# Kernel tuning notes

Hardware: AMD Instinct MI355X
Metric: run time of the kernel (lower is better)

## Reference

```python
import jax, jax.numpy as jnp
import numpy as np
from jax import lax

B, C_IN, IMG, P = 8, 320, 64, 2
H = W = IMG // P            # 32
N = H * W                   # 1024 tokens
DIM = 128 * P * P           # 512
DEPTH, HEADS, DH = 6, 8, 64
INNER = HEADS * DH          # 512
MLP = 512
EPS = 1e-5


def layernorm(x, g, b):
    mu = x.mean(-1, keepdims=True)
    var = ((x - mu) ** 2).mean(-1, keepdims=True)
    return (x - mu) * lax.rsqrt(var + EPS) * g + b


def conv3x3(x, w, b):
    y = lax.conv_general_dilated(x, w, (1, 1), 'SAME',
                                 dimension_numbers=('NCHW', 'OIHW', 'NCHW'))
    return y + b[None, :, None, None]


def posemb_sincos_2d(h, w, dim, temperature=10000.0):
    y, x = jnp.meshgrid(jnp.arange(h, dtype=jnp.float32),
                        jnp.arange(w, dtype=jnp.float32), indexing='ij')
    omega = jnp.arange(dim // 4, dtype=jnp.float32) / (dim // 4 - 1)
    omega = 1.0 / (temperature ** omega)
    y = y.reshape(-1)[:, None] * omega[None, :]
    x = x.reshape(-1)[:, None] * omega[None, :]
    return jnp.concatenate([jnp.sin(x), jnp.cos(x), jnp.sin(y), jnp.cos(y)], axis=1)


def prepare_attn_mask(mask):
    # attn mask allows position pairs where either row or col token is marked.
    f = 64 // H
    m = (mask == 1)
    r = m.reshape(-1, H, f, W, f).any(axis=(2, 4)).reshape(-1, N)  # [M, N] bool
    return r[:, :, None] | r[:, None, :]                            # [M, N, N]


def setup_inputs() -> dict:
    key = jax.random.key(0)
    ks = jax.random.split(key, 24)
    s = 0.02
    d = dict(
        img=jax.random.normal(ks[0], (B, C_IN, IMG, IMG), jnp.float32),
        mask=jax.random.randint(ks[1], (DEPTH * B, 64, 64), 0, 2, jnp.int32),
        conv1_w=jax.random.normal(ks[2], (128, C_IN, 3, 3), jnp.float32) * s,
        conv1_b=jnp.zeros((128,), jnp.float32),
        ln_p_g=jnp.ones((DIM,), jnp.float32), ln_p_b=jnp.zeros((DIM,), jnp.float32),
        proj_w=jax.random.normal(ks[3], (DIM, DIM), jnp.float32) * s,
        proj_b=jnp.zeros((DIM,), jnp.float32),
        ln_q_g=jnp.ones((DIM,), jnp.float32), ln_q_b=jnp.zeros((DIM,), jnp.float32),
        attn_ln_g=jnp.ones((DEPTH, DIM), jnp.float32),
        attn_ln_b=jnp.zeros((DEPTH, DIM), jnp.float32),
        wqkv=jax.random.normal(ks[4], (DEPTH, DIM, 3 * INNER), jnp.float32) * s,
        wo=jax.random.normal(ks[5], (DEPTH, INNER, DIM), jnp.float32) * s,
        ff_ln_g=jnp.ones((DEPTH, DIM), jnp.float32),
        ff_ln_b=jnp.zeros((DEPTH, DIM), jnp.float32),
        w1=jax.random.normal(ks[6], (DEPTH, DIM, MLP), jnp.float32) * s,
        b1=jnp.zeros((DEPTH, MLP), jnp.float32),
        w2=jax.random.normal(ks[7], (DEPTH, MLP, DIM), jnp.float32) * s,
        b2=jnp.zeros((DEPTH, DIM), jnp.float32),
        conv2_w=jax.random.normal(ks[8], (C_IN, 128, 3, 3), jnp.float32) * s,
        conv2_b=jnp.zeros((C_IN,), jnp.float32),
    )
    return d


def reference(img, mask, conv1_w, conv1_b, ln_p_g, ln_p_b, proj_w, proj_b,
              ln_q_g, ln_q_b, attn_ln_g, attn_ln_b, wqkv, wo,
              ff_ln_g, ff_ln_b, w1, b1, w2, b2, conv2_w, conv2_b):
    am = prepare_attn_mask(mask).reshape(DEPTH, B, N, N)  # per-layer masks

    # patch embed: conv -> rearrange 'b c (h p1) (w p2) -> b (h w) (p1 p2 c)'
    y = conv3x3(img, conv1_w, conv1_b)                           # [B,128,64,64]
    y = y.reshape(B, 128, H, P, W, P).transpose(0, 2, 4, 3, 5, 1)
    y = y.reshape(B, N, P * P * 128)                             # [B,N,512]
    x = layernorm(y, ln_p_g, ln_p_b) @ proj_w + proj_b
    x = layernorm(x, ln_q_g, ln_q_b)
    x = x + posemb_sincos_2d(H, W, DIM).astype(x.dtype)

    scale = DH ** -0.5
    for i in range(DEPTH):
        xn = layernorm(x, attn_ln_g[i], attn_ln_b[i])
        qkv = xn @ wqkv[i]                                       # [B,N,3*INNER]
        q, k, v = jnp.split(qkv, 3, axis=-1)
        q, k, v = (t.reshape(B, N, HEADS, DH).transpose(0, 2, 1, 3)
                   for t in (q, k, v))
        dots = jnp.einsum('bhid,bhjd->bhij', q, k) * scale
        min_val = lax.stop_gradient(dots.min())
        dots = jnp.where(am[i][:, None, :, :], dots, min_val)
        attn = jax.nn.softmax(dots, axis=-1)
        o = jnp.einsum('bhij,bhjd->bhid', attn, v)
        o = o.transpose(0, 2, 1, 3).reshape(B, N, INNER) @ wo[i]
        x = o + x
        h = layernorm(x, ff_ln_g[i], ff_ln_b[i]) @ w1[i] + b1[i]
        x = jax.nn.gelu(h, approximate=False) @ w2[i] + b2[i] + x

    # 'b (h w) (p1 p2 c) -> b c (h p1) (w p2)' then conv
    z = x.reshape(B, H, W, P, P, 128).transpose(0, 5, 1, 3, 2, 4)
    z = z.reshape(B, 128, IMG, IMG)
    return conv3x3(z, conv2_w, conv2_b)
```

## Files before the change

### kernel.cpp

```cpp
#include <hip/hip_runtime.h>
#include <hip/hip_bf16.h>
#include <math.h>

typedef __attribute__((ext_vector_type(8))) short short8;
typedef __attribute__((ext_vector_type(4))) float f32x4;
typedef unsigned short u16;
typedef unsigned int u32;

#define DEV __device__ __forceinline__

DEV float bf2f(u16 u){ u32 x = ((u32)u)<<16; return __builtin_bit_cast(float, x); }
DEV u16 f2bf(float f){ u32 x = __builtin_bit_cast(u32, f); return (u16)((x + 0x7FFFu + ((x>>16)&1u))>>16); }
DEV f32x4 mfma16(short8 a, short8 b, f32x4 c){ return __builtin_amdgcn_mfma_f32_16x16x32_bf16(a,b,c,0,0,0); }
DEV void gload16(const void* g, void* l){
  __builtin_amdgcn_global_load_lds((const __attribute__((address_space(1))) void*)g,
                                   (__attribute__((address_space(3))) void*)l, 16, 0, 0);
}
DEV u32 fkey(float f){ u32 b = __builtin_bit_cast(u32, f); return (b & 0x80000000u) ? ~b : (b ^ 0x80000000u); }
DEV float funkey(u32 k){ u32 b = (k & 0x80000000u) ? (k ^ 0x80000000u) : ~k; return __builtin_bit_cast(float, b); }

static constexpr size_t O_PROJW = 0;
static constexpr size_t O_QKVW  = O_PROJW + 524288;
static constexpr size_t O_WOW   = O_QKVW + 9437184;
static constexpr size_t O_W1W   = O_WOW + 3145728;
static constexpr size_t O_W2W   = O_W1W + 3145728;
static constexpr size_t O_C1W   = O_W2W + 3145728;
static constexpr size_t O_C2W   = O_C1W + 737280;
static constexpr size_t O_RA    = O_C2W + 737280;
static constexpr size_t O_RB    = O_RA + 22302720;
static constexpr size_t O_X     = O_RB + 25165824;
static constexpr size_t O_D     = O_X + 16777216;
static constexpr size_t O_F     = O_D + 8388608;
static constexpr size_t O_RM    = O_F + 8388608;
static constexpr size_t O_MIN   = O_RM + 49152;
static constexpr size_t WS_NEED = O_MIN + 256;

__global__ __launch_bounds__(256) void k_transpose_bf(const float* __restrict__ src, u16* __restrict__ dst, int K, int N){
  __shared__ float tile[32][33];
  const int k0 = blockIdx.x*32, n0 = blockIdx.y*32;
  src += (size_t)blockIdx.z*K*N; dst += (size_t)blockIdx.z*K*N;
  const int c = threadIdx.x & 31, r4 = threadIdx.x >> 5;
  for(int r=r4; r<32; r+=8) tile[r][c] = src[(size_t)(k0+r)*N + n0+c];
  __syncthreads();
  for(int r=r4; r<32; r+=8) dst[(size_t)(n0+r)*K + k0+c] = f2bf(tile[c][r]);
}

__global__ __launch_bounds__(256) void k_convw(const float* __restrict__ src, u16* __restrict__ dst, int OC, int IC){
  int idx = blockIdx.x*256 + threadIdx.x;
  int total = OC*IC*9;
  if(idx >= total) return;
  int oc = idx/(IC*9); int rem = idx - oc*IC*9; int tap = rem/IC; int ic = rem - tap*IC;
  dst[idx] = f2bf(src[(size_t)(oc*IC+ic)*9 + tap]);
}

__global__ __launch_bounds__(256) void k_pad_img(const float* __restrict__ img, u16* __restrict__ pcl){
  const int by = blockIdx.x; const int b = by>>6, y = by&63; const int c0 = blockIdx.y*64;
  __shared__ float t[64][65];
  const int tx = threadIdx.x & 63, tz = threadIdx.x >> 6;
  for(int ci=tz; ci<64; ci+=4) t[ci][tx] = img[(((size_t)b*320 + c0+ci)*64 + y)*64 + tx];
  __syncthreads();
  for(int x=tz; x<64; x+=4) pcl[(((size_t)b*66 + y+1)*66 + (x+1))*320 + c0 + tx] = f2bf(t[tx][x]);
}

__global__ __launch_bounds__(256) void k_pad_tok(const float* __restrict__ x, u16* __restrict__ pcl){
  int idx = blockIdx.x*256 + threadIdx.x;
  const int c = idx & 127; int r = idx >> 7; const int xx = r & 63; r >>= 6; const int yy = r & 63; const int b = r >> 6;
  const int n = (yy>>1)*32 + (xx>>1); const int f = (yy&1)*256 + (xx&1)*128 + c;
  pcl[(((size_t)b*66 + yy+1)*66 + xx+1)*128 + c] = f2bf(x[((size_t)b*1024 + n)*512 + f]);
}

__global__ __launch_bounds__(256) void k_rmask(const int* __restrict__ mask, unsigned char* __restrict__ rm){
  int idx = blockIdx.x*256 + threadIdx.x;
  if(idx >= 48*1024) return;
  const int m = idx >> 10, n = idx & 1023; const int h = n>>5, w = n&31;
  const int* mp = mask + ((size_t)m*64 + h*2)*64 + w*2;
  rm[idx] = (unsigned char)((mp[0]==1) | (mp[1]==1) | (mp[64]==1) | (mp[65]==1));
}

__global__ __launch_bounds__(256) void k_vt(const u16* __restrict__ v, u16* __restrict__ vt){
  const int nt = blockIdx.x, bh = blockIdx.y;
  __shared__ u16 t[64][72];
  const int tid = threadIdx.x;
  const int i = tid>>2, cq = tid&3;
  const u16* src = v + ((size_t)bh*1024 + nt*64 + i)*64 + cq*16;
  const short8 s0 = *(const short8*)src;
  const short8 s1 = *(const short8*)(src+8);
  #pragma unroll
  for(int e=0;e<8;e++){ t[cq*16+e][i] = (u16)s0[e]; t[cq*16+8+e][i] = (u16)s1[e]; }
  __syncthreads();
  short8 o0, o1;
  #pragma unroll
  for(int e=0;e<8;e++){ o0[e] = (short)t[i][cq*16+e]; o1[e] = (short)t[i][cq*16+8+e]; }
  u16* dst = vt + (size_t)bh*65536 + (size_t)i*1024 + nt*64 + cq*16;
  *(short8*)dst = o0;
  *(short8*)(dst+8) = o1;
}

__global__ __launch_bounds__(256) void k_ln_bf(const float* __restrict__ in, const float* __restrict__ gw,
                                               const float* __restrict__ bw, u16* __restrict__ out){
  const int tok = blockIdx.x*4 + (threadIdx.x>>6);
  const int lane = threadIdx.x & 63;
  const float* rp = in + (size_t)tok*512 + lane*8;
  const float4 a = *(const float4*)rp;
  const float4 b = *(const float4*)(rp+4);
  float s  = a.x+a.y+a.z+a.w + b.x+b.y+b.z+b.w;
  float sq = a.x*a.x+a.y*a.y+a.z*a.z+a.w*a.w + b.x*b.x+b.y*b.y+b.z*b.z+b.w*b.w;
  #pragma unroll
  for(int off=1; off<64; off<<=1){ s += __shfl_xor(s,off); sq += __shfl_xor(sq,off); }
  const float mu = s*(1.f/512.f);
  const float rs = rsqrtf(fmaxf(sq*(1.f/512.f) - mu*mu, 0.f) + 1e-5f);
  const float4 g0 = *(const float4*)(gw + lane*8);
  const float4 g1 = *(const float4*)(gw + lane*8 + 4);
  const float4 b0 = *(const float4*)(bw + lane*8);
  const float4 b1 = *(const float4*)(bw + lane*8 + 4);
  short8 o8;
  o8[0]=f2bf((a.x-mu)*rs*g0.x+b0.x); o8[1]=f2bf((a.y-mu)*rs*g0.y+b0.y);
  o8[2]=f2bf((a.z-mu)*rs*g0.z+b0.z); o8[3]=f2bf((a.w-mu)*rs*g0.w+b0.w);
  o8[4]=f2bf((b.x-mu)*rs*g1.x+b1.x); o8[5]=f2bf((b.y-mu)*rs*g1.y+b1.y);
  o8[6]=f2bf((b.z-mu)*rs*g1.z+b1.z); o8[7]=f2bf((b.w-mu)*rs*g1.w+b1.w);
  *(short8*)(out + (size_t)tok*512 + lane*8) = o8;
}

__global__ __launch_bounds__(256) void k_lnq_pos(const float* __restrict__ in, const float* __restrict__ gw,
                                                 const float* __restrict__ bw, float* __restrict__ out){
  const int tok = blockIdx.x*4 + (threadIdx.x>>6);
  const int lane = threadIdx.x & 63;
  const float* rp = in + (size_t)tok*512 + lane*8;
  const float4 a = *(const float4*)rp;
  const float4 b = *(const float4*)(rp+4);
  float s  = a.x+a.y+a.z+a.w + b.x+b.y+b.z+b.w;
  float sq = a.x*a.x+a.y*a.y+a.z*a.z+a.w*a.w + b.x*b.x+b.y*b.y+b.z*b.z+b.w*b.w;
  #pragma unroll
  for(int off=1; off<64; off<<=1){ s += __shfl_xor(s,off); sq += __shfl_xor(sq,off); }
  const float mu = s*(1.f/512.f);
  const float rs = rsqrtf(fmaxf(sq*(1.f/512.f) - mu*mu, 0.f) + 1e-5f);
  const int n = tok & 1023; const int yy = n>>5, xx = n&31;
  const int f0 = lane*8; const int sec = f0>>7;
  const float coord = (sec<2) ? (float)xx : (float)yy;
  const float vv[8] = {a.x,a.y,a.z,a.w,b.x,b.y,b.z,b.w};
  float ov[8];
  #pragma unroll
  for(int j=0;j<8;j++){
    const int f = f0+j; const int qq = f & 127;
    const float om = __expf(-(float)qq * (9.2103403719761836f/127.f));
    const float arg = coord * om;
    const float pe = (sec&1) ? __cosf(arg) : __sinf(arg);
    ov[j] = (vv[j]-mu)*rs*gw[f] + bw[f] + pe;
  }
  float* op = out + (size_t)tok*512 + f0;
  *(float4*)op = (float4){ov[0],ov[1],ov[2],ov[3]};
  *(float4*)(op+4) = (float4){ov[4],ov[5],ov[6],ov[7]};
}

template<int EPI, int CONVC>
__global__ __launch_bounds__(256, 4)
void k_gemm(const u16* __restrict__ A, const u16* __restrict__ Wt,
            const float* __restrict__ bias, void* __restrict__ outp,
            const float* __restrict__ resid, int M, int N, int Kd)
{
  __shared__ u16 Ald[2][4096];
  __shared__ u16 Bld[2][4096];
  const int tid = threadIdx.x, lane = tid & 63, wv = tid >> 6;
  const int lr = lane & 15, g = lane >> 4;
  const int m0 = blockIdx.x * 64, n0 = blockIdx.y * 64;
  const int wm = (wv >> 1) * 32, wn = (wv & 1) * 32;
  const int srow = tid >> 3;
  const int sc  = (tid & 7) ^ (srow & 7);
  int b0=0, yy0=0;
  if constexpr (CONVC != 0){ b0 = m0>>12; yy0 = (m0>>6)&63; }
  const u16* arow0p; const u16* arow1p;
  if constexpr (CONVC != 0){
    arow0p = A; arow1p = A;
  } else {
    arow0p = A + (size_t)(m0+srow)*Kd + sc*8;
    arow1p = A + (size_t)(m0+srow+32)*Kd + sc*8;
  }
  const u16* brow0p = Wt + (size_t)(n0+srow)*Kd + sc*8;
  const u16* brow1p = Wt + (size_t)(n0+srow+32)*Kd + sc*8;

  f32x4 acc[2][2];
  #pragma unroll
  for(int i=0;i<2;i++)
    #pragma unroll
    for(int j=0;j<2;j++) acc[i][j] = (f32x4){0.f,0.f,0.f,0.f};

  const int nIter = Kd >> 6;
  int cur = 0;

  auto stage = [&](int kt, int buf){
    const int k0 = kt << 6;
    const u16 *ga0, *ga1;
    if constexpr (CONVC != 0){
      const int tap = k0 / CONVC;
      const int ic0 = k0 - tap*CONVC;
      const int ky = tap/3, kx = tap - 3*(tap/3);
      const size_t rb0 = ((size_t)((b0*66 + yy0+ky)*66 + kx))*CONVC + ic0 + sc*8;
      ga0 = A + rb0 + (size_t)(srow)*CONVC;
      ga1 = A + rb0 + (size_t)(srow+32)*CONVC;
    } else {
      ga0 = arow0p + k0;
      ga1 = arow1p + k0;
    }
    gload16(ga0, &Ald[buf][tid*8]);
    gload16(ga1, &Ald[buf][2048 + tid*8]);
    gload16(brow0p + k0, &Bld[buf][tid*8]);
    gload16(brow1p + k0, &Bld[buf][2048 + tid*8]);
  };

  stage(0, 0);
  for(int kt=0; kt<nIter; ++kt){
    __syncthreads();
    if(kt+1 < nIter) stage(kt+1, cur^1);
    short8 af[2][2], bg[2][2];
    #pragma unroll
    for(int mi=0;mi<2;mi++)
      #pragma unroll
      for(int kk=0;kk<2;kk++){
        const int R = wm + mi*16 + lr;
        const int Rn = wn + mi*16 + lr;
        const int c = kk*4 + g;
        af[mi][kk] = *(const short8*)&Ald[cur][R*64 + ((c ^ (R&7))<<3)];
        bg[mi][kk] = *(const short8*)&Bld[cur][Rn*64 + ((c ^ (Rn&7))<<3)];
      }
    #pragma unroll
    for(int mi=0;mi<2;mi++)
      #pragma unroll
      for(int nj=0;nj<2;nj++)
        #pragma unroll
        for(int kk=0;kk<2;kk++)
          acc[mi][nj] = mfma16(af[mi][kk], bg[nj][kk], acc[mi][nj]);
    cur ^= 1;
  }

  #pragma unroll
  for(int mi=0;mi<2;mi++){
    #pragma unroll
    for(int nj=0;nj<2;nj++){
      #pragma unroll
      for(int r=0;r<4;r++){
        const int mrow = m0 + wm + mi*16 + g*4 + r;
        const int ncol = n0 + wn + nj*16 + lr;
        float val = acc[mi][nj][r];
        if constexpr (EPI==0 || EPI==3 || EPI==4 || EPI==5 || EPI==6)
          val += bias[ncol];
        if constexpr (EPI==0){
          ((float*)outp)[(size_t)mrow*512 + ncol] = val;
        } else if constexpr (EPI==1){
          const int sec = ncol >> 9, rem = ncol & 511;
          const int head = rem >> 6, d = rem & 63;
          const int b = mrow >> 10, t = mrow & 1023;
          ((u16*)outp)[(size_t)sec*4194304 + ((size_t)((b*8+head)*1024 + t))*64 + d] = f2bf(val);
        } else if constexpr (EPI==2 || EPI==4){
          const size_t idx = (size_t)mrow*512 + ncol;
          ((float*)outp)[idx] = resid[idx] + val;
        } else if constexpr (EPI==3){
          const float gl = 0.5f * val * (1.f + erff(val * 0.70710678118654752f));
          ((u16*)outp)[(size_t)mrow*512 + ncol] = f2bf(gl);
        } else if constexpr (EPI==5){
          const int b = mrow>>12; const int rr = mrow&4095; const int y = rr>>6; const int xx = rr&63;
          const size_t pidx = ((size_t)(b*1024 + (y>>1)*32 + (xx>>1)))*512 + (y&1)*256 + (xx&1)*128 + ncol;
          ((float*)outp)[pidx] = val;
        } else if constexpr (EPI==6){
          const int b = mrow>>12; const int rr = mrow&4095; const int y = rr>>6; const int xx = rr&63;
          ((float*)outp)[(((size_t)(b*320 + ncol))*64 + y)*64 + xx] = val;
        }
      }
    }
  }
}

__global__ __launch_bounds__(256, 4)
void k_attn_minmax(const u16* __restrict__ q, const u16* __restrict__ k, u32* __restrict__ keys, int layer){
  const int id = blockIdx.x;
  const int qt = (id>>3)&15;
  const int bh = ((id&7)<<3) | (id>>7);
  __shared__ u16 Kld[2][4096];
  __shared__ float redn[4], redx[4];
  const int tid = threadIdx.x, lane = tid & 63, wv = tid >> 6;
  const int lr = lane & 15, g = lane >> 4;
  const u16* qp = q + ((size_t)bh*1024 + qt*64 + wv*16 + lr)*64;
  const short8 qa0 = *(const short8*)(qp + g*8);
  const short8 qa1 = *(const short8*)(qp + 32 + g*8);
  const u16* kbase = k + (size_t)bh*65536;
  const int srow = tid>>3, scs = lane&7;
  const int scg = scs ^ (srow&7);
  const int srow2 = srow + 32;
  const int scg2 = scs ^ (srow2&7);
  float mn = 3.0e38f, mx = -3.0e38f;
  gload16(kbase + (size_t)srow*64 + scg*8, &Kld[0][wv*512]);
  gload16(kbase + (size_t)srow2*64 + scg2*8, &Kld[0][2048 + wv*512]);
  int cur = 0;
  for(int jt=0; jt<16; ++jt){
    __syncthreads();
    if(jt < 15){
      const int j1 = (jt+1)*64;
      gload16(kbase + (size_t)(j1+srow)*64 + scg*8, &Kld[cur^1][wv*512]);
      gload16(kbase + (size_t)(j1+srow2)*64 + scg2*8, &Kld[cur^1][2048 + wv*512]);
    }
    #pragma unroll
    for(int c=0;c<4;c++){
      const int rr = c*16 + lr;
      const short8 kb0 = *(const short8*)&Kld[cur][rr*64 + ((g ^ (rr&7))<<3)];
      const short8 kb1 = *(const short8*)&Kld[cur][rr*64 + (((g+4) ^ (rr&7))<<3)];
      f32x4 s4 = (f32x4){0.f,0.f,0.f,0.f};
      s4 = mfma16(qa0, kb0, s4);
      s4 = mfma16(qa1, kb1, s4);
      mn = fminf(mn, fminf(fminf(s4[0],s4[1]), fminf(s4[2],s4[3])));
      mx = fmaxf(mx, fmaxf(fmaxf(s4[0],s4[1]), fmaxf(s4[2],s4[3])));
    }
    cur ^= 1;
  }
  mn *= 0.125f; mx *= 0.125f;
  #pragma unroll
  for(int off=32; off; off>>=1){
    mn = fminf(mn, __shfl_down(mn, off));
    mx = fmaxf(mx, __shfl_down(mx, off));
  }
  if(lane==0){ redn[wv] = mn; redx[wv] = mx; }
  __syncthreads();
  if(tid==0){
    atomicMin(keys + layer,     fkey(fminf(fminf(redn[0],redn[1]), fminf(redn[2],redn[3]))));
    atomicMax(keys + 8 + layer, fkey(fmaxf(fmaxf(redx[0],redx[1]), fmaxf(redx[2],redx[3]))));
  }
}

__global__ __launch_bounds__(256, 4)
void k_attn(const u16* __restrict__ q, const u16* __restrict__ k, const u16* __restrict__ vt,
            const unsigned char* __restrict__ rm, const u32* __restrict__ keys,
            u16* __restrict__ o, int layer){
  const int id = blockIdx.x;
  const int qt = (id>>3)&15;
  const int bh = ((id&7)<<3) | (id>>7);
  const int b = bh>>3, h = bh&7;
  __shared__ u16 Kld[2][4096];
  __shared__ u16 Vtld[2][4096];
  __shared__ u16 Pld[4][1024];
  const int tid = threadIdx.x, lane = tid & 63, wv = tid >> 6;
  const int lr = lane & 15, g = lane >> 4;
  const u16* qp = q + ((size_t)bh*1024 + qt*64 + wv*16 + lr)*64;
  const short8 qa0 = *(const short8*)(qp + g*8);
  const short8 qa1 = *(const short8*)(qp + 32 + g*8);
  const float L2E = 1.44269504088896f;
  const float SC = 0.125f * L2E;
  float mnv = funkey(keys[layer]);
  float mxv = funkey(keys[8+layer]);
  if(!(mnv >= -1e38f && mnv <= 1e38f)) mnv = 0.f;
  if(!(mxv >= -1e38f && mxv <= 1e38f)) mxv = 0.f;
  const float minvE = mnv * L2E;
  const float ME    = mxv * L2E;
  const unsigned char* rmp = rm + (size_t)(layer*8 + b)*1024;
  bool rrow[4];
  #pragma unroll
  for(int r=0;r<4;r++) rrow[r] = rmp[qt*64 + wv*16 + g*4 + r] != 0;
  float lrun[4] = {0.f,0.f,0.f,0.f};
  f32x4 accd[4];
  #pragma unroll
  for(int d=0;d<4;d++) accd[d] = (f32x4){0.f,0.f,0.f,0.f};
  const u16* kbase = k + (size_t)bh*65536;
  const u16* vtbase = vt + (size_t)bh*65536;
  const int srow = tid>>3, scs = lane&7;
  const int scg = scs ^ (srow&7);
  const int srow2 = srow + 32;
  const int scg2 = scs ^ (srow2&7);
  gload16(kbase + (size_t)srow*64 + scg*8, &Kld[0][wv*512]);
  gload16(kbase + (size_t)srow2*64 + scg2*8, &Kld[0][2048 + wv*512]);
  gload16(vtbase + (size_t)srow*1024 + scg*8, &Vtld[0][wv*512]);
  gload16(vtbase + (size_t)srow2*1024 + scg2*8, &Vtld[0][2048 + wv*512]);
  int cur = 0;
  for(int jt=0; jt<16; ++jt){
    const int j0 = jt*64;
    __syncthreads();
    if(jt < 15){
      const int j1 = j0 + 64;
      gload16(kbase + (size_t)(j1+srow)*64 + scg*8, &Kld[cur^1][wv*512]);
      gload16(kbase + (size_t)(j1+srow2)*64 + scg2*8, &Kld[cur^1][2048 + wv*512]);
      gload16(vtbase + (size_t)srow*1024 + j1 + scg*8, &Vtld[cur^1][wv*512]);
      gload16(vtbase + (size_t)srow2*1024 + j1 + scg2*8, &Vtld[cur^1][2048 + wv*512]);
    }
    float p4[4][4];
    #pragma unroll
    for(int c=0;c<4;c++){
      const int rr = c*16 + lr;
      const short8 kb0 = *(const short8*)&Kld[cur][rr*64 + ((g ^ (rr&7))<<3)];
      const short8 kb1 = *(const short8*)&Kld[cur][rr*64 + (((g+4) ^ (rr&7))<<3)];
      f32x4 s4 = (f32x4){0.f,0.f,0.f,0.f};
      s4 = mfma16(qa0, kb0, s4);
      s4 = mfma16(qa1, kb1, s4);
      const bool colok = rmp[j0 + rr] != 0;
      #pragma unroll
      for(int r=0;r<4;r++){
        const float vl = (rrow[r] | colok) ? s4[r]*SC : minvE;
        p4[c][r] = exp2f(fmaxf(vl - ME, -120.f));
      }
    }
    #pragma unroll
    for(int r=0;r<4;r++)
      lrun[r] += (p4[0][r]+p4[1][r]) + (p4[2][r]+p4[3][r]);
    #pragma unroll
    for(int c=0;c<4;c++)
      #pragma unroll
      for(int r=0;r<4;r++){
        const int ql = g*4+r, cl = c*16+lr;
        Pld[wv][ql*64 + ((((cl>>3) ^ (ql&7))<<3) | (cl&7))] = f2bf(p4[c][r]);
      }
    asm volatile("s_waitcnt lgkmcnt(0)" ::: "memory");
    __builtin_amdgcn_sched_barrier(0);
    const short8 pa0 = *(const short8*)&Pld[wv][lr*64 + ((g ^ (lr&7))<<3)];
    const short8 pa1 = *(const short8*)&Pld[wv][lr*64 + (((g+4) ^ (lr&7))<<3)];
    #pragma unroll
    for(int d=0;d<4;d++){
      const int rr = d*16 + lr;
      const short8 vb0 = *(const short8*)&Vtld[cur][rr*64 + ((g ^ (rr&7))<<3)];
      const short8 vb1 = *(const short8*)&Vtld[cur][rr*64 + (((g+4) ^ (rr&7))<<3)];
      accd[d] = mfma16(pa0, vb0, accd[d]);
      accd[d] = mfma16(pa1, vb1, accd[d]);
    }
    cur ^= 1;
  }
  float inv[4];
  #pragma unroll
  for(int r=0;r<4;r++){
    float ls = lrun[r];
    ls += __shfl_xor(ls,1); ls += __shfl_xor(ls,2);
    ls += __shfl_xor(ls,4); ls += __shfl_xor(ls,8);
    inv[r] = 1.f / ls;
  }
  #pragma unroll
  for(int d=0;d<4;d++)
    #pragma unroll
    for(int r=0;r<4;r++){
      const int qrow = qt*64 + wv*16 + g*4 + r;
      o[((size_t)b*1024 + qrow)*512 + h*64 + d*16 + lr] = f2bf(accd[d][r] * inv[r]);
    }
}

extern "C" void kernel_launch(void* const* d_in, const int* in_sizes, int n_in,
                              void* d_out, int out_size, void* d_ws, size_t ws_size,
                              hipStream_t stream)
{
  const float* img     = (const float*)d_in[0];
  const int*   mask    = (const int*)d_in[1];
  const float* conv1_w = (const float*)d_in[2];
  const float* conv1_b = (const float*)d_in[3];
  const float* ln_p_g  = (const float*)d_in[4];
  const float* ln_p_b  = (const float*)d_in[5];
  const float* proj_w  = (const float*)d_in[6];
  const float* proj_b  = (const float*)d_in[7];
  const float* ln_q_g  = (const float*)d_in[8];
  const float* ln_q_b  = (const float*)d_in[9];
  const float* attn_ln_g = (const float*)d_in[10];
  const float* attn_ln_b = (const float*)d_in[11];
  const float* wqkv    = (const float*)d_in[12];
  const float* wo      = (const float*)d_in[13];
  const float* ff_ln_g = (const float*)d_in[14];
  const float* ff_ln_b = (const float*)d_in[15];
  const float* w1      = (const float*)d_in[16];
  const float* b1      = (const float*)d_in[17];
  const float* w2      = (const float*)d_in[18];
  const float* b2      = (const float*)d_in[19];
  const float* conv2_w = (const float*)d_in[20];
  const float* conv2_b = (const float*)d_in[21];

  if(ws_size < WS_NEED) return;
  char* ws = (char*)d_ws;
  u16* projWt = (u16*)(ws + O_PROJW);
  u16* qkvWt  = (u16*)(ws + O_QKVW);
  u16* woWt   = (u16*)(ws + O_WOW);
  u16* w1Wt   = (u16*)(ws + O_W1W);
  u16* w2Wt   = (u16*)(ws + O_W2W);
  u16* c1Wt   = (u16*)(ws + O_C1W);
  u16* c2Wt   = (u16*)(ws + O_C2W);
  u16* pcl    = (u16*)(ws + O_RA);
  float* tmpf = (float*)(ws + O_RA);
  u16* vtb    = (u16*)(ws + O_RA);
  float* patches = (float*)(ws + O_RB);
  u16* qkvb   = (u16*)(ws + O_RB);
  float* xbuf = (float*)(ws + O_X);
  u16* xnbf   = (u16*)(ws + O_D);
  u16* obf    = (u16*)(ws + O_F);
  unsigned char* rmb = (unsigned char*)(ws + O_RM);
  u32* minbuf = (u32*)(ws + O_MIN);

  hipMemsetAsync(ws + O_MIN, 0xFF, 32, stream);
  hipMemsetAsync(ws + O_MIN + 32, 0, 32, stream);
  hipMemsetAsync(ws + O_RA, 0, 22302720, stream);

  k_transpose_bf<<<dim3(16,16,1),256,0,stream>>>(proj_w, projWt, 512, 512);
  k_transpose_bf<<<dim3(16,48,6),256,0,stream>>>(wqkv,   qkvWt,  512, 1536);
  k_transpose_bf<<<dim3(16,16,6),256,0,stream>>>(wo,     woWt,   512, 512);
  k_transpose_bf<<<dim3(16,16,6),256,0,stream>>>(w1,     w1Wt,   512, 512);
  k_transpose_bf<<<dim3(16,16,6),256,0,stream>>>(w2,     w2Wt,   512, 512);
  k_convw<<<1440,256,0,stream>>>(conv1_w, c1Wt, 128, 320);
  k_convw<<<1440,256,0,stream>>>(conv2_w, c2Wt, 320, 128);
  k_rmask<<<192,256,0,stream>>>(mask, rmb);

  k_pad_img<<<dim3(512,5),256,0,stream>>>(img, pcl);
  k_gemm<5,320><<<dim3(512,2),256,0,stream>>>(pcl, c1Wt, conv1_b, patches, nullptr, 32768, 128, 2880);
  k_ln_bf<<<2048,256,0,stream>>>(patches, ln_p_g, ln_p_b, xnbf);
  k_gemm<0,0><<<dim3(128,8),256,0,stream>>>(xnbf, projWt, proj_b, tmpf, nullptr, 8192, 512, 512);
  k_lnq_pos<<<2048,256,0,stream>>>(tmpf, ln_q_g, ln_q_b, xbuf);

  const u16* qb = qkvb;
  const u16* kb = qkvb + 4194304;
  const u16* vb = qkvb + 8388608;
  for(int i=0;i<6;i++){
    k_ln_bf<<<2048,256,0,stream>>>(xbuf, attn_ln_g + i*512, attn_ln_b + i*512, xnbf);
    k_gemm<1,0><<<dim3(128,24),256,0,stream>>>(xnbf, qkvWt + (size_t)i*1536*512, nullptr, qkvb, nullptr, 8192, 1536, 512);
    k_vt<<<dim3(16,64),256,0,stream>>>(vb, vtb);
    k_attn_minmax<<<1024,256,0,stream>>>(qb, kb, minbuf, i);
    k_attn<<<1024,256,0,stream>>>(qb, kb, vtb, rmb, minbuf, obf, i);
    k_gemm<2,0><<<dim3(128,8),256,0,stream>>>(obf, woWt + (size_t)i*512*512, nullptr, xbuf, xbuf, 8192, 512, 512);
    k_ln_bf<<<2048,256,0,stream>>>(xbuf, ff_ln_g + i*512, ff_ln_b + i*512, xnbf);
    k_gemm<3,0><<<dim3(128,8),256,0,stream>>>(xnbf, w1Wt + (size_t)i*512*512, b1 + i*512, obf, nullptr, 8192, 512, 512);
    k_gemm<4,0><<<dim3(128,8),256,0,stream>>>(obf, w2Wt + (size_t)i*512*512, b2 + i*512, xbuf, xbuf, 8192, 512, 512);
  }

  hipMemsetAsync(ws + O_RA, 0, 8921088, stream);
  k_pad_tok<<<16384,256,0,stream>>>(xbuf, pcl);
  k_gemm<6,128><<<dim3(512,5),256,0,stream>>>(pcl, c2Wt, conv2_b, d_out, nullptr, 32768, 320, 1152);
}
```

Baseline: 1.070 ms.

## Use bit-packed row masks and transposed QK^T MFMA in attention softmax

The token mask is packed into 64-bit ballot words, so the attention kernel reads column and row validity as bits instead of per-element byte loads. The QK^T MFMA operands are swapped so each lane holds a query row across key columns. This lets the row sum be accumulated in a single scalar and lets P be written to LDS as packed bf16 pairs via v_cvt_pk_bf16_f32. s_setprio is raised around the MFMAs in both attention kernels. The changes are meant to cut mask loads, scalar converts and LDS stores in the softmax inner loop, at the cost of trickier lane/swizzle indexing that must stay consistent with the PV MFMA layout.

```diff
diff --git a/kernel.cpp b/kernel.cpp
--- a/kernel.cpp
+++ b/kernel.cpp
@@ -6,6 +6,7 @@
 typedef __attribute__((ext_vector_type(4))) float f32x4;
 typedef unsigned short u16;
 typedef unsigned int u32;
+typedef unsigned long long u64;
 
 #define DEV __device__ __forceinline__
 
@@ -18,6 +19,7 @@
 }
 DEV u32 fkey(float f){ u32 b = __builtin_bit_cast(u32, f); return (b & 0x80000000u) ? ~b : (b ^ 0x80000000u); }
 DEV float funkey(u32 k){ u32 b = (k & 0x80000000u) ? (k ^ 0x80000000u) : ~k; return __builtin_bit_cast(float, b); }
+DEV u32 cvtpk(float lo, float hi){ u32 d; asm("v_cvt_pk_bf16_f32 %0, %1, %2" : "=v"(d) : "v"(lo), "v"(hi)); return d; }
 
 static constexpr size_t O_PROJW = 0;
 static constexpr size_t O_QKVW  = O_PROJW + 524288;
@@ -33,7 +35,8 @@
 static constexpr size_t O_F     = O_D + 8388608;
 static constexpr size_t O_RM    = O_F + 8388608;
 static constexpr size_t O_MIN   = O_RM + 49152;
-static constexpr size_t WS_NEED = O_MIN + 256;
+static constexpr size_t O_RMB   = O_MIN + 256;
+static constexpr size_t WS_NEED = O_RMB + 8192;
 
 __global__ __launch_bounds__(256) void k_transpose_bf(const float* __restrict__ src, u16* __restrict__ dst, int K, int N){
   __shared__ float tile[32][33];
@@ -69,12 +72,15 @@
   pcl[(((size_t)b*66 + yy+1)*66 + xx+1)*128 + c] = f2bf(x[((size_t)b*1024 + n)*512 + f]);
 }
 
-__global__ __launch_bounds__(256) void k_rmask(const int* __restrict__ mask, unsigned char* __restrict__ rm){
+__global__ __launch_bounds__(256) void k_rmask(const int* __restrict__ mask, unsigned char* __restrict__ rm,
+                                               u64* __restrict__ rmbits){
   int idx = blockIdx.x*256 + threadIdx.x;
-  if(idx >= 48*1024) return;
   const int m = idx >> 10, n = idx & 1023; const int h = n>>5, w = n&31;
   const int* mp = mask + ((size_t)m*64 + h*2)*64 + w*2;
-  rm[idx] = (unsigned char)((mp[0]==1) | (mp[1]==1) | (mp[64]==1) | (mp[65]==1));
+  const int v = (mp[0]==1) | (mp[1]==1) | (mp[64]==1) | (mp[65]==1);
+  rm[idx] = (unsigned char)v;
+  const u64 bm = __ballot(v);
+  if((threadIdx.x & 63) == 0) rmbits[idx>>6] = bm;
 }
 
 __global__ __launch_bounds__(256) void k_vt(const u16* __restrict__ v, u16* __restrict__ vt){
@@ -303,8 +309,10 @@
       const short8 kb0 = *(const short8*)&Kld[cur][rr*64 + ((g ^ (rr&7))<<3)];
       const short8 kb1 = *(const short8*)&Kld[cur][rr*64 + (((g+4) ^ (rr&7))<<3)];
       f32x4 s4 = (f32x4){0.f,0.f,0.f,0.f};
+      __builtin_amdgcn_s_setprio(1);
       s4 = mfma16(qa0, kb0, s4);
       s4 = mfma16(qa1, kb1, s4);
+      __builtin_amdgcn_s_setprio(0);
       mn = fminf(mn, fminf(fminf(s4[0],s4[1]), fminf(s4[2],s4[3])));
       mx = fmaxf(mx, fmaxf(fmaxf(s4[0],s4[1]), fmaxf(s4[2],s4[3])));
     }
@@ -326,7 +334,7 @@
 
 __global__ __launch_bounds__(256, 4)
 void k_attn(const u16* __restrict__ q, const u16* __restrict__ k, const u16* __restrict__ vt,
-            const unsigned char* __restrict__ rm, const u32* __restrict__ keys,
+            const u64* __restrict__ rmbits, const u32* __restrict__ keys,
             u16* __restrict__ o, int layer){
   const int id = blockIdx.x;
   const int qt = (id>>3)&15;
@@ -334,9 +342,10 @@
   const int b = bh>>3, h = bh&7;
   __shared__ u16 Kld[2][4096];
   __shared__ u16 Vtld[2][4096];
-  __shared__ u16 Pld[4][1024];
+  __shared__ u32 Pld[4][512];
   const int tid = threadIdx.x, lane = tid & 63, wv = tid >> 6;
   const int lr = lane & 15, g = lane >> 4;
+  const int L7 = lr & 7;
   const u16* qp = q + ((size_t)bh*1024 + qt*64 + wv*16 + lr)*64;
   const short8 qa0 = *(const short8*)(qp + g*8);
   const short8 qa1 = *(const short8*)(qp + 32 + g*8);
@@ -346,13 +355,23 @@
   float mxv = funkey(keys[8+layer]);
   if(!(mnv >= -1e38f && mnv <= 1e38f)) mnv = 0.f;
   if(!(mxv >= -1e38f && mxv <= 1e38f)) mxv = 0.f;
-  const float minvE = mnv * L2E;
-  const float ME    = mxv * L2E;
-  const unsigned char* rmp = rm + (size_t)(layer*8 + b)*1024;
-  bool rrow[4];
-  #pragma unroll
-  for(int r=0;r<4;r++) rrow[r] = rmp[qt*64 + wv*16 + g*4 + r] != 0;
-  float lrun[4] = {0.f,0.f,0.f,0.f};
+  const float ME   = mxv * L2E;
+  const float minM = fmaxf(mnv*L2E - ME, -120.f);
+  const u32* cbp = (const u32*)(rmbits + (size_t)(layer*8 + b)*16);
+  const u32 qbitw = cbp[qt*2 + ((wv*16+lr)>>5)];
+  const u32 rfill = ((qbitw >> ((wv*16+lr)&31)) & 1u) ? 0xFu : 0u;
+  u32* Pw = &Pld[wv][0];
+  u32 wslot[4][2];
+  #pragma unroll
+  for(int c=0;c<4;c++){
+    const int blk = c*2 + (g>>1);
+    wslot[c][0] = lr*32 + ((blk ^ L7)<<2) + (g&1)*2;
+    wslot[c][1] = wslot[c][0] + 1;
+  }
+  const u32 ra0 = lr*32 + ((g ^ L7)<<2);
+  const u32 ra1 = lr*32 + (((4+g) ^ L7)<<2);
+
+  float lsum = 0.f;
   f32x4 accd[4];
   #pragma unroll
   for(int d=0;d<4;d++) accd[d] = (f32x4){0.f,0.f,0.f,0.f};
@@ -368,63 +387,58 @@
   gload16(vtbase + (size_t)srow2*1024 + scg2*8, &Vtld[0][2048 + wv*512]);
   int cur = 0;
   for(int jt=0; jt<16; ++jt){
-    const int j0 = jt*64;
     __syncthreads();
     if(jt < 15){
-      const int j1 = j0 + 64;
+      const int j1 = (jt+1)*64;
       gload16(kbase + (size_t)(j1+srow)*64 + scg*8, &Kld[cur^1][wv*512]);
       gload16(kbase + (size_t)(j1+srow2)*64 + scg2*8, &Kld[cur^1][2048 + wv*512]);
       gload16(vtbase + (size_t)srow*1024 + j1 + scg*8, &Vtld[cur^1][wv*512]);
       gload16(vtbase + (size_t)srow2*1024 + j1 + scg2*8, &Vtld[cur^1][2048 + wv*512]);
     }
-    float p4[4][4];
+    const u32 cb_lo = cbp[jt*2], cb_hi = cbp[jt*2+1];
     #pragma unroll
     for(int c=0;c<4;c++){
       const int rr = c*16 + lr;
       const short8 kb0 = *(const short8*)&Kld[cur][rr*64 + ((g ^ (rr&7))<<3)];
       const short8 kb1 = *(const short8*)&Kld[cur][rr*64 + (((g+4) ^ (rr&7))<<3)];
       f32x4 s4 = (f32x4){0.f,0.f,0.f,0.f};
-      s4 = mfma16(qa0, kb0, s4);
-      s4 = mfma16(qa1, kb1, s4);
-      const bool colok = rmp[j0 + rr] != 0;
+      __builtin_amdgcn_s_setprio(1);
+      s4 = mfma16(kb0, qa0, s4);
+      s4 = mfma16(kb1, qa1, s4);
+      __builtin_amdgcn_s_setprio(0);
+      const u32 cw = (((c<2) ? cb_lo : cb_hi) >> ((c&1)*16 + g*4)) | rfill;
+      float e[4];
       #pragma unroll
       for(int r=0;r<4;r++){
-        const float vl = (rrow[r] | colok) ? s4[r]*SC : minvE;
-        p4[c][r] = exp2f(fmaxf(vl - ME, -120.f));
+        float sv = fmaxf(fmaf(s4[r], SC, -ME), -120.f);
+        const float vl = ((cw >> r) & 1u) ? sv : minM;
+        e[r] = exp2f(vl);
+        lsum += e[r];
       }
-    }
-    #pragma unroll
-    for(int r=0;r<4;r++)
-      lrun[r] += (p4[0][r]+p4[1][r]) + (p4[2][r]+p4[3][r]);
-    #pragma unroll
-    for(int c=0;c<4;c++)
-      #pragma unroll
-      for(int r=0;r<4;r++){
-        const int ql = g*4+r, cl = c*16+lr;
-        Pld[wv][ql*64 + ((((cl>>3) ^ (ql&7))<<3) | (cl&7))] = f2bf(p4[c][r]);
-      }
+      Pw[wslot[c][0]] = cvtpk(e[0], e[1]);
+      Pw[wslot[c][1]] = cvtpk(e[2], e[3]);
+    }
     asm volatile("s_waitcnt lgkmcnt(0)" ::: "memory");
     __builtin_amdgcn_sched_barrier(0);
-    const short8 pa0 = *(const short8*)&Pld[wv][lr*64 + ((g ^ (lr&7))<<3)];
-    const short8 pa1 = *(const short8*)&Pld[wv][lr*64 + (((g+4) ^ (lr&7))<<3)];
+    const short8 pa0 = *(const short8*)&Pw[ra0];
+    const short8 pa1 = *(const short8*)&Pw[ra1];
     #pragma unroll
     for(int d=0;d<4;d++){
       const int rr = d*16 + lr;
       const short8 vb0 = *(const short8*)&Vtld[cur][rr*64 + ((g ^ (rr&7))<<3)];
       const short8 vb1 = *(const short8*)&Vtld[cur][rr*64 + (((g+4) ^ (rr&7))<<3)];
+      __builtin_amdgcn_s_setprio(1);
       accd[d] = mfma16(pa0, vb0, accd[d]);
       accd[d] = mfma16(pa1, vb1, accd[d]);
+      __builtin_amdgcn_s_setprio(0);
     }
     cur ^= 1;
   }
+  lsum += __shfl_xor(lsum, 16);
+  lsum += __shfl_xor(lsum, 32);
   float inv[4];
   #pragma unroll
-  for(int r=0;r<4;r++){
-    float ls = lrun[r];
-    ls += __shfl_xor(ls,1); ls += __shfl_xor(ls,2);
-    ls += __shfl_xor(ls,4); ls += __shfl_xor(ls,8);
-    inv[r] = 1.f / ls;
-  }
+  for(int r=0;r<4;r++) inv[r] = 1.f / __shfl(lsum, g*4 + r);
   #pragma unroll
   for(int d=0;d<4;d++)
     #pragma unroll
@@ -480,6 +494,7 @@
   u16* obf    = (u16*)(ws + O_F);
   unsigned char* rmb = (unsigned char*)(ws + O_RM);
   u32* minbuf = (u32*)(ws + O_MIN);
+  u64* rmbits = (u64*)(ws + O_RMB);
 
   hipMemsetAsync(ws + O_MIN, 0xFF, 32, stream);
   hipMemsetAsync(ws + O_MIN + 32, 0, 32, stream);
@@ -492,7 +507,7 @@
   k_transpose_bf<<<dim3(16,16,6),256,0,stream>>>(w2,     w2Wt,   512, 512);
   k_convw<<<1440,256,0,stream>>>(conv1_w, c1Wt, 128, 320);
   k_convw<<<1440,256,0,stream>>>(conv2_w, c2Wt, 320, 128);
-  k_rmask<<<192,256,0,stream>>>(mask, rmb);
+  k_rmask<<<192,256,0,stream>>>(mask, rmb, rmbits);
 
   k_pad_img<<<dim3(512,5),256,0,stream>>>(img, pcl);
   k_gemm<5,320><<<dim3(512,2),256,0,stream>>>(pcl, c1Wt, conv1_b, patches, nullptr, 32768, 128, 2880);
@@ -508,7 +523,7 @@
     k_gemm<1,0><<<dim3(128,24),256,0,stream>>>(xnbf, qkvWt + (size_t)i*1536*512, nullptr, qkvb, nullptr, 8192, 1536, 512);
     k_vt<<<dim3(16,64),256,0,stream>>>(vb, vtb);
     k_attn_minmax<<<1024,256,0,stream>>>(qb, kb, minbuf, i);
-    k_attn<<<1024,256,0,stream>>>(qb, kb, vtb, rmb, minbuf, obf, i);
+    k_attn<<<1024,256,0,stream>>>(qb, kb, vtb, rmbits, minbuf, obf, i);
     k_gemm<2,0><<<dim3(128,8),256,0,stream>>>(obf, woWt + (size_t)i*512*512, nullptr, xbuf, xbuf, 8192, 512, 512);
     k_ln_bf<<<2048,256,0,stream>>>(xbuf, ff_ln_g + i*512, ff_ln_b + i*512, xnbf);
     k_gemm<3,0><<<dim3(128,8),256,0,stream>>>(xnbf, w1Wt + (size_t)i*512*512, b1 + i*512, obf, nullptr, 8192, 512, 512);
```

Result: faster. 1.043 ms (-2.6%).
